# Performance work log

Measured on AMD Instinct MI355X. Metric: run time of the kernel, lower is better.

## Reference

```python
import jax, jax.numpy as jnp
import numpy as np


def setup_inputs() -> dict:
    key = jax.random.key(0)
    k1, k2 = jax.random.split(key)
    qs = jax.random.normal(k1, (64, 32, 128), dtype=jnp.float32)   # (n_queries, n_query_tokens, dim)
    ps = jax.random.normal(k2, (64, 1024, 128), dtype=jnp.float32)  # (n_docs, n_doc_tokens, dim)
    return {"qs": qs, "ps": ps}


def reference(qs, ps):
    # ColBERT MaxSim: for each (query b, doc c), sum over query tokens of the
    # max similarity against all doc tokens.
    # scores[b,c,n,s] = sum_d qs[b,n,d] * ps[c,s,d]
    sim = jnp.einsum('bnd,csd->bcns', qs, ps)  # (n_q, n_d, tok_q, tok_d)
    scores = sim.max(axis=3).sum(axis=2)       # (n_q, n_d)
    return scores
```

## Files before the change

kernel.cpp:

```cpp
#include <hip/hip_runtime.h>
#include <stdint.h>


typedef __bf16 bf16x8 __attribute__((ext_vector_type(8)));
typedef float floatx16 __attribute__((ext_vector_type(16)));

union FU { bf16x8 v; uint4 u; };

__device__ inline bf16x8 cvt8(const float4& a, const float4& b) {
  bf16x8 r;
  r[0] = (__bf16)a.x; r[1] = (__bf16)a.y; r[2] = (__bf16)a.z; r[3] = (__bf16)a.w;
  r[4] = (__bf16)b.x; r[5] = (__bf16)b.y; r[6] = (__bf16)b.z; r[7] = (__bf16)b.w;
  return r;
}

__device__ inline float rmax16(const floatx16& a) {
  float m0 = fmaxf(fmaxf(a[0], a[1]), fmaxf(a[2], a[3]));
  float m1 = fmaxf(fmaxf(a[4], a[5]), fmaxf(a[6], a[7]));
  float m2 = fmaxf(fmaxf(a[8], a[9]), fmaxf(a[10], a[11]));
  float m3 = fmaxf(fmaxf(a[12], a[13]), fmaxf(a[14], a[15]));
  return fmaxf(fmaxf(m0, m1), fmaxf(m2, m3));
}

typedef __attribute__((address_space(1))) const void gas_t;
typedef __attribute__((address_space(3))) void las_t;
__device__ inline void gload_lds16f(const float* g, float* l) {
  __builtin_amdgcn_global_load_lds((gas_t*)g, (las_t*)l, 16, 0, 0);
}

#define ZERO16 {0, 0, 0, 0, 0, 0, 0, 0, 0, 0, 0, 0, 0, 0, 0, 0}

__global__ __launch_bounds__(256) void maxsim_kernel(const float* __restrict__ qs,
                                                     const float* __restrict__ ps,
                                                     float* __restrict__ out) {
  const int lane = threadIdx.x & 63;
  const int wave = threadIdx.x >> 6;

  const int xcd = blockIdx.x & 7;
  const int slot = blockIdx.x >> 3;
  const int c = xcd * 8 + (slot >> 3);
  const int bg = slot & 7;
  const int qb0 = bg * 8 + wave * 2;

  const int row = lane & 31;
  const int hi8 = (lane >> 5) * 8;

  uint4 qf[2][8];
#pragma unroll
  for (int bb = 0; bb < 2; ++bb) {
    const float* q = qs + ((qb0 + bb) * 32 + row) * 128 + hi8;
#pragma unroll
    for (int k = 0; k < 8; ++k) {
      float4 a = *(const float4*)(q + k * 16);
      float4 b = *(const float4*)(q + k * 16 + 4);
      FU f; f.v = cvt8(a, b);
      qf[bb][k] = f.u;
    }
  }
#pragma unroll
  for (int bb = 0; bb < 2; ++bb)
#pragma unroll
    for (int k = 0; k < 8; ++k)
      asm volatile("" : "+v"(qf[bb][k].x), "+v"(qf[bb][k].y),
                        "+v"(qf[bb][k].z), "+v"(qf[bb][k].w));

  __shared__ __align__(16) float lds_p[3][4096];

  const int pg_lane = (c * 1024 + row) * 128 + hi8;

#define STAGE(L, tt)                                                          \
  _Pragma("unroll") for (int jj = 0; jj < 4; ++jj) {                          \
    const int m = wave * 4 + jj;                                              \
    const int j = m >> 1, h = m & 1;                                          \
    gload_lds16f(ps + pg_lane + (tt) * 4096 + j * 16 + h * 4,                 \
                 (L) + m * 256);                                              \
  }

  float* pA = &lds_p[0][0];
  float* pB = &lds_p[1][0];
  float* pC = &lds_p[2][0];

  STAGE(pA, 0)
  STAGE(pB, 1)
  asm volatile("s_waitcnt vmcnt(4)" ::: "memory");
  __builtin_amdgcn_s_barrier();

  float vmax0 = -3.4e38f, vmax1 = -3.4e38f;

#pragma unroll 1
  for (int t = 0; t < 32; ++t) {
    if (t + 2 < 32) {
      STAGE(pC, t + 2)
    }
    const float* lp = pA + lane * 4;
    floatx16 acc0 = ZERO16, acc1 = ZERO16;
#pragma unroll
    for (int k = 0; k < 8; ++k) {
      float4 lo = *(const float4*)(lp + (2 * k) * 256);
      float4 hi = *(const float4*)(lp + (2 * k + 1) * 256);
      bf16x8 af = cvt8(lo, hi);
      FU f0; f0.u = qf[0][k];
      FU f1; f1.u = qf[1][k];
      acc0 = __builtin_amdgcn_mfma_f32_32x32x16_bf16(af, f0.v, acc0, 0, 0, 0);
      acc1 = __builtin_amdgcn_mfma_f32_32x32x16_bf16(af, f1.v, acc1, 0, 0, 0);
    }
    vmax0 = fmaxf(vmax0, rmax16(acc0));
    vmax1 = fmaxf(vmax1, rmax16(acc1));
    if (t + 2 < 32) {
      asm volatile("s_waitcnt vmcnt(4)" ::: "memory");
    } else if (t + 1 < 32) {
      asm volatile("s_waitcnt vmcnt(0)" ::: "memory");
    }
    if (t + 1 < 32) __builtin_amdgcn_s_barrier();
    float* tmp = pA; pA = pB; pB = pC; pC = tmp;
  }

  vmax0 = fmaxf(vmax0, __shfl_xor(vmax0, 32, 64));
  vmax1 = fmaxf(vmax1, __shfl_xor(vmax1, 32, 64));
#pragma unroll
  for (int o = 16; o > 0; o >>= 1) {
    vmax0 += __shfl_xor(vmax0, o, 64);
    vmax1 += __shfl_xor(vmax1, o, 64);
  }
  if (lane == 0) {
    out[(qb0 + 0) * 64 + c] = vmax0;
    out[(qb0 + 1) * 64 + c] = vmax1;
  }
}

extern "C" void kernel_launch(void* const* d_in, const int* in_sizes, int n_in,
                              void* d_out, int out_size, void* d_ws, size_t ws_size,
                              hipStream_t stream) {
  const float* qs = (const float*)d_in[0];
  const float* ps = (const float*)d_in[1];
  float* out = (float*)d_out;
  (void)d_ws; (void)ws_size;

  maxsim_kernel<<<dim3(512), dim3(256), 0, stream>>>(qs, ps, out);
}
```

Baseline: 127.1 us.

## Convert doc tiles to bf16 once before LDS and double-buffer through registers

Replaces the direct global-to-LDS fp32 loads with register-staged loads. Each block converts its doc tile to bf16 once and writes it to a double-buffered LDS tile, and every step now covers 64 doc tokens instead of 32. Before, each of the four waves re-converted the same fp32 data from LDS, so this cuts LDS read volume and repeated conversion work. In exchange it adds register pressure for the staged loads and can expose global-load latency because the pipeline is now only two deep.

```diff
diff --git a/kernel.cpp b/kernel.cpp
--- a/kernel.cpp
+++ b/kernel.cpp
@@ -20,12 +20,6 @@
   float m2 = fmaxf(fmaxf(a[8], a[9]), fmaxf(a[10], a[11]));
   float m3 = fmaxf(fmaxf(a[12], a[13]), fmaxf(a[14], a[15]));
   return fmaxf(fmaxf(m0, m1), fmaxf(m2, m3));
-}
-
-typedef __attribute__((address_space(1))) const void gas_t;
-typedef __attribute__((address_space(3))) void las_t;
-__device__ inline void gload_lds16f(const float* g, float* l) {
-  __builtin_amdgcn_global_load_lds((gas_t*)g, (las_t*)l, 16, 0, 0);
 }
 
 #define ZERO16 {0, 0, 0, 0, 0, 0, 0, 0, 0, 0, 0, 0, 0, 0, 0, 0}
@@ -64,55 +58,61 @@
       asm volatile("" : "+v"(qf[bb][k].x), "+v"(qf[bb][k].y),
                         "+v"(qf[bb][k].z), "+v"(qf[bb][k].w));
 
-  __shared__ __align__(16) float lds_p[3][4096];
+  __shared__ __align__(16) ushort lds_p[2][8192];
 
-  const int pg_lane = (c * 1024 + row) * 128 + hi8;
+  const float* pg = ps + (c * 1024 + row) * 128 + hi8;
 
-#define STAGE(L, tt)                                                          \
+  float4 F[8];
+
+#define STAGE_LOAD(tt)                                                        \
   _Pragma("unroll") for (int jj = 0; jj < 4; ++jj) {                          \
     const int m = wave * 4 + jj;                                              \
-    const int j = m >> 1, h = m & 1;                                          \
-    gload_lds16f(ps + pg_lane + (tt) * 4096 + j * 16 + h * 4,                 \
-                 (L) + m * 256);                                              \
+    const int u = m >> 3, j = m & 7;                                          \
+    const float* src = pg + (tt) * 8192 + u * 32 * 128 + j * 16;              \
+    F[2 * jj] = *(const float4*)src;                                          \
+    F[2 * jj + 1] = *(const float4*)(src + 4);                                \
   }
 
-  float* pA = &lds_p[0][0];
-  float* pB = &lds_p[1][0];
-  float* pC = &lds_p[2][0];
+#define STAGE_WRITE(B)                                                        \
+  _Pragma("unroll") for (int jj = 0; jj < 4; ++jj) {                          \
+    const int m = wave * 4 + jj;                                              \
+    const int u = m >> 3, j = m & 7;                                          \
+    *(bf16x8*)(&(B)[u * 4096 + j * 512 + lane * 8]) =                         \
+        cvt8(F[2 * jj], F[2 * jj + 1]);                                       \
+  }
 
-  STAGE(pA, 0)
-  STAGE(pB, 1)
-  asm volatile("s_waitcnt vmcnt(4)" ::: "memory");
-  __builtin_amdgcn_s_barrier();
+  STAGE_LOAD(0)
+  STAGE_WRITE(lds_p[0])
+  __syncthreads();
 
   float vmax0 = -3.4e38f, vmax1 = -3.4e38f;
+  int cb = 0;
 
 #pragma unroll 1
-  for (int t = 0; t < 32; ++t) {
-    if (t + 2 < 32) {
-      STAGE(pC, t + 2)
+  for (int t = 0; t < 16; ++t) {
+    if (t < 15) {
+      STAGE_LOAD(t + 1)
     }
-    const float* lp = pA + lane * 4;
-    floatx16 acc0 = ZERO16, acc1 = ZERO16;
+    const ushort* lp = &lds_p[cb][0] + lane * 8;
 #pragma unroll
-    for (int k = 0; k < 8; ++k) {
-      float4 lo = *(const float4*)(lp + (2 * k) * 256);
-      float4 hi = *(const float4*)(lp + (2 * k + 1) * 256);
-      bf16x8 af = cvt8(lo, hi);
-      FU f0; f0.u = qf[0][k];
-      FU f1; f1.u = qf[1][k];
-      acc0 = __builtin_amdgcn_mfma_f32_32x32x16_bf16(af, f0.v, acc0, 0, 0, 0);
-      acc1 = __builtin_amdgcn_mfma_f32_32x32x16_bf16(af, f1.v, acc1, 0, 0, 0);
+    for (int u = 0; u < 2; ++u) {
+      floatx16 acc0 = ZERO16, acc1 = ZERO16;
+#pragma unroll
+      for (int k = 0; k < 8; ++k) {
+        bf16x8 af = *(const bf16x8*)(lp + u * 4096 + k * 512);
+        FU f0; f0.u = qf[0][k];
+        FU f1; f1.u = qf[1][k];
+        acc0 = __builtin_amdgcn_mfma_f32_32x32x16_bf16(af, f0.v, acc0, 0, 0, 0);
+        acc1 = __builtin_amdgcn_mfma_f32_32x32x16_bf16(af, f1.v, acc1, 0, 0, 0);
+      }
+      vmax0 = fmaxf(vmax0, rmax16(acc0));
+      vmax1 = fmaxf(vmax1, rmax16(acc1));
     }
-    vmax0 = fmaxf(vmax0, rmax16(acc0));
-    vmax1 = fmaxf(vmax1, rmax16(acc1));
-    if (t + 2 < 32) {
-      asm volatile("s_waitcnt vmcnt(4)" ::: "memory");
-    } else if (t + 1 < 32) {
-      asm volatile("s_waitcnt vmcnt(0)" ::: "memory");
+    if (t < 15) {
+      STAGE_WRITE(lds_p[cb ^ 1])
     }
-    if (t + 1 < 32) __builtin_amdgcn_s_barrier();
-    float* tmp = pA; pA = pB; pB = pC; pC = tmp;
+    __syncthreads();
+    cb ^= 1;
   }
 
   vmax0 = fmaxf(vmax0, __shfl_xor(vmax0, 32, 64));
```

New measurement: 111.3 us. -12.4%, faster.
